# Kernel optimization log

Measured on AMD Instinct MI355X. Metric: run time of the kernel, lower is better.

## Reference

```python
import jax, jax.numpy as jnp
import numpy as np

N_NODES = 100000
N_EDGES = 1600000
IN_DIM = 128
OUT_DIM = 32
NUM_HEADS = 4


def setup_inputs() -> dict:
    key = jax.random.key(0)
    k1, k2, k3, k4, k5, k6 = jax.random.split(key, 6)
    feat = jax.random.normal(k1, (N_NODES, IN_DIM), dtype=jnp.float32)
    # xavier-uniform-ish scales
    fc_w = jax.random.normal(k2, (OUT_DIM * NUM_HEADS, IN_DIM), dtype=jnp.float32) * (1.0 / np.sqrt(IN_DIM))
    attn_src = jax.random.normal(k3, (1, NUM_HEADS, OUT_DIM), dtype=jnp.float32) * 0.1
    attn_dst = jax.random.normal(k4, (1, NUM_HEADS, OUT_DIM), dtype=jnp.float32) * 0.1
    src = jax.random.randint(k5, (N_EDGES,), 0, N_NODES, dtype=jnp.int64)
    dst = jax.random.randint(k6, (N_EDGES,), 0, N_NODES, dtype=jnp.int64)
    return {"feat": feat, "fc_w": fc_w, "attn_src": attn_src, "attn_dst": attn_dst, "src": src, "dst": dst}


def reference(feat, fc_w, attn_src, attn_dst, src, dst):
    N = feat.shape[0]
    # fc: [N, H*D] -> [N, H, D]
    h = (feat @ fc_w.T).reshape(N, NUM_HEADS, OUT_DIM)
    # per-node attention logits [N, H]
    e_src = jnp.sum(h * attn_src, axis=-1)
    e_dst = jnp.sum(h * attn_dst, axis=-1)
    # per-edge logits, LeakyReLU(0.2)  [E, H]
    e = e_src[src] + e_dst[dst]
    e = jnp.where(e > 0, e, 0.2 * e)
    # edge softmax over incoming edges of each dst node
    m = jax.ops.segment_max(e, dst, num_segments=N)          # [N, H], -inf for empty
    a = jnp.exp(e - m[dst])                                  # [E, H]
    s = jax.ops.segment_sum(a, dst, num_segments=N)          # [N, H]
    a = a / jnp.where(s[dst] > 0, s[dst], 1.0)
    # weighted scatter-sum aggregation: u_mul_e + sum
    msg = h[src] * a[:, :, None]                             # [E, H, D]
    out = jax.ops.segment_sum(msg, dst, num_segments=N)      # [N, H, D]
    h_out = out.reshape(N, NUM_HEADS * OUT_DIM)
    # residual: in_dim == out_dim*num_heads -> identity residual
    return h_out + feat
```

## Files before the change

### kernel.cpp

```cpp
#include <hip/hip_runtime.h>

#define HD 128
#define NHEADS 4
#define MBLK 128
#define APITCH 136

#define CHUNK_SHIFT 8
#define CHUNK_NODES 256
#define MAXCH 512
#define CLCAP 4352
#define PT_EDGES 4096
#define EPT 16
#define CAP 48

#define H8_SCALE   15.875f
#define H8_INVSCALE 0.062992126f

typedef __attribute__((ext_vector_type(8))) short bf16x8;
typedef __attribute__((ext_vector_type(4))) float f32x4;

__device__ __forceinline__ unsigned short f2bf(float x) {
    union { float f; unsigned u; } a; a.f = x;
    unsigned r = a.u + 0x7fffu + ((a.u >> 16) & 1u);
    return (unsigned short)(r >> 16);
}

__global__ __launch_bounds__(256) void partition_edges(
    const int* __restrict__ src, const int* __restrict__ dst,
    int* __restrict__ cursor,
    int2* __restrict__ clist,
    int2* __restrict__ spillP, int* __restrict__ nspillP,
    int E, int nchunks, int spillPCap)
{
    __shared__ int lcnt[MAXCH];
    __shared__ int gbase[MAXCH];
    const int tid = threadIdx.x;
    for (int i = tid; i < MAXCH; i += 256) lcnt[i] = 0;
    __syncthreads();

    const int e0 = blockIdx.x * PT_EDGES + tid;
    int d[EPT], s[EPT], r[EPT];
#pragma unroll
    for (int k = 0; k < EPT; k++) {
        int e = e0 + k * 256;
        d[k] = 0; s[k] = 0; r[k] = 0;
        if (e < E) { d[k] = dst[e]; s[k] = src[e]; }
    }
#pragma unroll
    for (int k = 0; k < EPT; k++) {
        int e = e0 + k * 256;
        if (e < E) r[k] = atomicAdd(&lcnt[d[k] >> CHUNK_SHIFT], 1);
    }
    __syncthreads();
    for (int c = tid; c < nchunks; c += 256) {
        int cnt = lcnt[c];
        gbase[c] = cnt ? atomicAdd(&cursor[c], cnt) : 0;
    }
    __syncthreads();
#pragma unroll
    for (int k = 0; k < EPT; k++) {
        int e = e0 + k * 256;
        if (e < E) {
            int c = d[k] >> CHUNK_SHIFT;
            int pos = gbase[c] + r[k];
            if (pos < CLCAP) {
                clist[(size_t)c * CLCAP + pos] = make_int2(d[k], s[k]);
            } else {
                int kk = atomicAdd(nspillP, 1);
                if (kk < spillPCap) spillP[kk] = make_int2(d[k], s[k]);
            }
        }
    }
}

__global__ __launch_bounds__(256) void bucketize(
    const int2* __restrict__ clist, const int* __restrict__ cursor,
    const int2* __restrict__ spillP, const int* __restrict__ nspillP,
    int* __restrict__ erec, int* __restrict__ counts,
    int2* __restrict__ spillB, int* __restrict__ nspillB,
    int N, int spillPCap, int spillBCap)
{
    __shared__ int lcnt[CHUNK_NODES];
    const int c = blockIdx.x;
    const int tid = threadIdx.x;
    lcnt[tid] = 0;
    __syncthreads();

    int cnt = cursor[c]; if (cnt > CLCAP) cnt = CLCAP;
    const int2* base = clist + (size_t)c * CLCAP;
    const int nodebase = c << CHUNK_SHIFT;

    for (int i = tid; i < cnt; i += 256) {
        int2 p = base[i];
        int pos = atomicAdd(&lcnt[p.x - nodebase], 1);
        if (pos < CAP) erec[(size_t)p.x * CAP + pos] = p.y;
        else { int kk = atomicAdd(nspillB, 1); if (kk < spillBCap) spillB[kk] = p; }
    }
    int nsp = *nspillP; if (nsp > spillPCap) nsp = spillPCap;
    for (int i = tid; i < nsp; i += 256) {
        int2 p = spillP[i];
        if ((p.x >> CHUNK_SHIFT) == c) {
            int pos = atomicAdd(&lcnt[p.x - nodebase], 1);
            if (pos < CAP) erec[(size_t)p.x * CAP + pos] = p.y;
            else { int kk = atomicAdd(nspillB, 1); if (kk < spillBCap) spillB[kk] = p; }
        }
    }
    __syncthreads();
    int n = nodebase + tid;
    if (n < N) counts[n] = lcnt[tid];
}

__global__ __launch_bounds__(256, 2) void gemm_mfma(
    const float* __restrict__ feat, const float* __restrict__ fc_w,
    const float* __restrict__ attn_src, const float* __restrict__ attn_dst,
    signed char* __restrict__ h8, float* __restrict__ e_src, float* __restrict__ e_dst,
    int N)
{
    __shared__ unsigned short As[MBLK * APITCH];
    __shared__ unsigned short Bs[HD * APITCH];
    const int tid = threadIdx.x;
    const int row0 = blockIdx.x * MBLK;

    for (int i = tid; i < 128 * 32; i += 256) {
        int o = i >> 5, j = i & 31;
        float4 v = ((const float4*)fc_w)[i];
        ushort4 u; u.x = f2bf(v.x); u.y = f2bf(v.y); u.z = f2bf(v.z); u.w = f2bf(v.w);
        *(ushort4*)&Bs[o * APITCH + j * 4] = u;
    }
    for (int i = tid; i < MBLK * 32; i += 256) {
        int r = i >> 5, j = i & 31;
        int rowg = row0 + r;
        float4 v = make_float4(0.f, 0.f, 0.f, 0.f);
        if (rowg < N) {
            v = ((const float4*)feat)[(size_t)rowg * 32 + j];
        }
        ushort4 u; u.x = f2bf(v.x); u.y = f2bf(v.y); u.z = f2bf(v.z); u.w = f2bf(v.w);
        *(ushort4*)&As[r * APITCH + j * 4] = u;
    }
    __syncthreads();

    const int w = tid >> 6, lane = tid & 63, quad = lane >> 4, lr = lane & 15;
    f32x4 acc[2][8];
#pragma unroll
    for (int rt = 0; rt < 2; rt++)
#pragma unroll
        for (int ct = 0; ct < 8; ct++) acc[rt][ct] = (f32x4){0.f, 0.f, 0.f, 0.f};

#pragma unroll
    for (int ks = 0; ks < 4; ks++) {
        const int k0 = ks * 32 + quad * 8;
        bf16x8 a0 = *(const bf16x8*)&As[(w * 32 + lr) * APITCH + k0];
        bf16x8 a1 = *(const bf16x8*)&As[(w * 32 + 16 + lr) * APITCH + k0];
        bf16x8 bf[8];
#pragma unroll
        for (int ct = 0; ct < 8; ct++)
            bf[ct] = *(const bf16x8*)&Bs[(ct * 16 + lr) * APITCH + k0];
#pragma unroll
        for (int ct = 0; ct < 8; ct++) {
            acc[0][ct] = __builtin_amdgcn_mfma_f32_16x16x32_bf16(a0, bf[ct], acc[0][ct], 0, 0, 0);
            acc[1][ct] = __builtin_amdgcn_mfma_f32_16x16x32_bf16(a1, bf[ct], acc[1][ct], 0, 0, 0);
        }
    }

#pragma unroll
    for (int rt = 0; rt < 2; rt++) {
#pragma unroll
        for (int ct = 0; ct < 8; ct++) {
            int col = ct * 16 + lr;
#pragma unroll
            for (int reg = 0; reg < 4; reg++) {
                int row = row0 + w * 32 + rt * 16 + quad * 4 + reg;
                if (row < N) {
                    float v = acc[rt][ct][reg];
                    v = fminf(fmaxf(v, -8.f), 8.f);
                    int q = (int)rintf(v * H8_SCALE);
                    h8[(size_t)row * 128 + col] = (signed char)q;
                }
            }
        }
    }

    float as_v[8], ad_v[8];
#pragma unroll
    for (int ct = 0; ct < 8; ct++) {
        as_v[ct] = attn_src[ct * 16 + lr];
        ad_v[ct] = attn_dst[ct * 16 + lr];
    }
#pragma unroll
    for (int rt = 0; rt < 2; rt++) {
#pragma unroll
        for (int reg = 0; reg < 4; reg++) {
            int row = row0 + w * 32 + rt * 16 + quad * 4 + reg;
            float ps[4], pd[4];
#pragma unroll
            for (int hd = 0; hd < 4; hd++) {
                ps[hd] = acc[rt][2 * hd][reg] * as_v[2 * hd] + acc[rt][2 * hd + 1][reg] * as_v[2 * hd + 1];
                pd[hd] = acc[rt][2 * hd][reg] * ad_v[2 * hd] + acc[rt][2 * hd + 1][reg] * ad_v[2 * hd + 1];
            }
#pragma unroll
            for (int off = 1; off < 16; off <<= 1) {
#pragma unroll
                for (int hd = 0; hd < 4; hd++) {
                    ps[hd] += __shfl_xor(ps[hd], off);
                    pd[hd] += __shfl_xor(pd[hd], off);
                }
            }
            if (lr == 0 && row < N) {
                *(float4*)&e_src[(size_t)row * 4] = make_float4(ps[0], ps[1], ps[2], ps[3]);
                *(float4*)&e_dst[(size_t)row * 4] = make_float4(pd[0], pd[1], pd[2], pd[3]);
            }
        }
    }
}

__global__ __launch_bounds__(256, 8) void node_agg(
    const int* __restrict__ erec, const int* __restrict__ counts,
    const signed char* __restrict__ h8,
    const float* __restrict__ e_src, const float* __restrict__ e_dst,
    const float* __restrict__ feat, float* __restrict__ out,
    const int2* __restrict__ spillB, const int* __restrict__ nspillB,
    int N, int spillBCap)
{
    const int lane  = threadIdx.x & 63;
    const int grp8  = lane >> 3;
    const int q     = lane & 7;
    const int head  = q >> 1;

    const int wgid   = (blockIdx.x * 256 + threadIdx.x) >> 6;
    const int nwaves = (gridDim.x * 256) >> 6;

    for (int nb0 = wgid * 8; nb0 < N; nb0 += nwaves * 8) {
        const int n = nb0 + grp8;
        const bool active = (n < N);
        const int deg = active ? counts[n] : 0;
        int md = deg;
        md = max(md, __shfl_xor(md, 8));
        md = max(md, __shfl_xor(md, 16));
        md = max(md, __shfl_xor(md, 32));
        if (md == 0) {
            if (active) {
                const float4* f = (const float4*)(feat + (size_t)n * HD) + q * 4;
                float4* o = (float4*)(out + (size_t)n * HD) + q * 4;
#pragma unroll
                for (int k = 0; k < 4; k++) o[k] = f[k];
            }
            continue;
        }
        const float ed = active ? e_dst[(size_t)n * 4 + head] : 0.f;
        const int fdeg = deg < CAP ? deg : CAP;
        const int mdc = md < CAP ? md : CAP;

        f32x4 a0 = (f32x4){0.f, 0.f, 0.f, 0.f};
        f32x4 a1 = (f32x4){0.f, 0.f, 0.f, 0.f};
        f32x4 a2 = (f32x4){0.f, 0.f, 0.f, 0.f};
        f32x4 a3 = (f32x4){0.f, 0.f, 0.f, 0.f};
        float s_l = 0.f;
#pragma unroll 4
        for (int j = 0; j < mdc; ++j) {
            float ev = 0.f; int si = 0;
            if (j < fdeg) {
                si = erec[(size_t)n * CAP + j];
                float v = e_src[(size_t)si * 4 + head] + ed;
                v = v > 0.f ? v : 0.2f * v;
                ev = __expf(v);
            }
            s_l += ev;
            const float evs = ev * H8_INVSCALE;
            uint4 hv = *(const uint4*)&h8[(size_t)si * 128 + q * 16];
            a0.x += evs * (float)(int)(signed char)(hv.x);
            a0.y += evs * (float)(int)(signed char)(hv.x >> 8);
            a0.z += evs * (float)(int)(signed char)(hv.x >> 16);
            a0.w += evs * (float)(int)(signed char)(hv.x >> 24);
            a1.x += evs * (float)(int)(signed char)(hv.y);
            a1.y += evs * (float)(int)(signed char)(hv.y >> 8);
            a1.z += evs * (float)(int)(signed char)(hv.y >> 16);
            a1.w += evs * (float)(int)(signed char)(hv.y >> 24);
            a2.x += evs * (float)(int)(signed char)(hv.z);
            a2.y += evs * (float)(int)(signed char)(hv.z >> 8);
            a2.z += evs * (float)(int)(signed char)(hv.z >> 16);
            a2.w += evs * (float)(int)(signed char)(hv.z >> 24);
            a3.x += evs * (float)(int)(signed char)(hv.w);
            a3.y += evs * (float)(int)(signed char)(hv.w >> 8);
            a3.z += evs * (float)(int)(signed char)(hv.w >> 16);
            a3.w += evs * (float)(int)(signed char)(hv.w >> 24);
        }
        if (__any(deg > CAP)) {
            int ns = *nspillB; if (ns > spillBCap) ns = spillBCap;
            for (int k = 0; k < ns; ++k) {
                int2 p = spillB[k];
                if (active && deg > CAP && p.x == n) {
                    int si = p.y;
                    float v = e_src[(size_t)si * 4 + head] + ed;
                    v = v > 0.f ? v : 0.2f * v;
                    float ev = __expf(v);
                    s_l += ev;
                    const float evs = ev * H8_INVSCALE;
                    uint4 hv = *(const uint4*)&h8[(size_t)si * 128 + q * 16];
                    a0.x += evs * (float)(int)(signed char)(hv.x);
                    a0.y += evs * (float)(int)(signed char)(hv.x >> 8);
                    a0.z += evs * (float)(int)(signed char)(hv.x >> 16);
                    a0.w += evs * (float)(int)(signed char)(hv.x >> 24);
                    a1.x += evs * (float)(int)(signed char)(hv.y);
                    a1.y += evs * (float)(int)(signed char)(hv.y >> 8);
                    a1.z += evs * (float)(int)(signed char)(hv.y >> 16);
                    a1.w += evs * (float)(int)(signed char)(hv.y >> 24);
                    a2.x += evs * (float)(int)(signed char)(hv.z);
                    a2.y += evs * (float)(int)(signed char)(hv.z >> 8);
                    a2.z += evs * (float)(int)(signed char)(hv.z >> 16);
                    a2.w += evs * (float)(int)(signed char)(hv.z >> 24);
                    a3.x += evs * (float)(int)(signed char)(hv.w);
                    a3.y += evs * (float)(int)(signed char)(hv.w >> 8);
                    a3.z += evs * (float)(int)(signed char)(hv.w >> 16);
                    a3.w += evs * (float)(int)(signed char)(hv.w >> 24);
                }
            }
        }
        if (active) {
            const float inv = (deg > 0) ? (1.0f / s_l) : 0.f;
            const float4* f = (const float4*)(feat + (size_t)n * HD) + q * 4;
            float4* o = (float4*)(out + (size_t)n * HD) + q * 4;
            float4 c0 = f[0], c1 = f[1], c2 = f[2], c3 = f[3];
            c0.x += a0.x * inv; c0.y += a0.y * inv; c0.z += a0.z * inv; c0.w += a0.w * inv;
            c1.x += a1.x * inv; c1.y += a1.y * inv; c1.z += a1.z * inv; c1.w += a1.w * inv;
            c2.x += a2.x * inv; c2.y += a2.y * inv; c2.z += a2.z * inv; c2.w += a2.w * inv;
            c3.x += a3.x * inv; c3.y += a3.y * inv; c3.z += a3.z * inv; c3.w += a3.w * inv;
            o[0] = c0; o[1] = c1; o[2] = c2; o[3] = c3;
        }
    }
}

extern "C" void kernel_launch(void* const* d_in, const int* in_sizes, int n_in,
                              void* d_out, int out_size, void* d_ws, size_t ws_size,
                              hipStream_t stream) {
    const float* feat     = (const float*)d_in[0];
    const float* fc_w     = (const float*)d_in[1];
    const float* attn_src = (const float*)d_in[2];
    const float* attn_dst = (const float*)d_in[3];
    const int*   src      = (const int*)d_in[4];
    const int*   dst      = (const int*)d_in[5];
    const int N = in_sizes[0] / HD;
    const int E = in_sizes[4];
    float* out = (float*)d_out;

    const int nchunks = (N + CHUNK_NODES - 1) >> CHUNK_SHIFT;
    const int spillPCap = E / 8;
    const int spillBCap = E / 8;

    signed char* h8 = (signed char*)d_ws;
    float* e_src  = (float*)(h8 + (size_t)N * HD);
    float* e_dst  = e_src + (size_t)N * NHEADS;
    int* erec     = (int*)(e_dst + (size_t)N * NHEADS);
    int* counts   = erec + (size_t)N * CAP;
    int* cursor   = counts + N;
    int* nspillP  = cursor + nchunks;
    int* nspillB  = nspillP + 1;
    int2* clist   = (int2*)(nspillB + 1);
    int2* spillP  = clist + (size_t)nchunks * CLCAP;
    int2* spillB  = spillP + spillPCap;

    const int npart = (E + PT_EDGES - 1) / PT_EDGES;

    hipMemsetAsync(cursor, 0, (size_t)(nchunks + 2) * sizeof(int), stream);
    partition_edges<<<npart, 256, 0, stream>>>(src, dst, cursor, clist, spillP, nspillP,
                                               E, nchunks, spillPCap);
    bucketize<<<nchunks, 256, 0, stream>>>(clist, cursor, spillP, nspillP,
                                           erec, counts, spillB, nspillB,
                                           N, spillPCap, spillBCap);
    gemm_mfma<<<(N + MBLK - 1) / MBLK, 256, 0, stream>>>(feat, fc_w, attn_src, attn_dst,
                                                         h8, e_src, e_dst, N);
    node_agg<<<2048, 256, 0, stream>>>(erec, counts, h8, e_src, e_dst, feat, out,
                                       spillB, nspillB, N, spillBCap);
}
```

Baseline: 272.2 us.

## Halve partition tile with LDS rank storage and widen bucketize to 512 threads

partition_edges now handles 2048 edges per block instead of 4096, doubling the block count. It keeps per-edge ranks in a shared-memory ushort array instead of registers, and reloads dst and src in the scatter phase instead of holding them in registers. bucketize now runs 512 threads per block and batches four loads before doing its atomics, to expose more memory-level parallelism across only about 391 blocks. The cost is re-reading the edge arrays, plus more global cursor atomics from the larger number of partition blocks.

```diff
diff --git a/kernel.cpp b/kernel.cpp
--- a/kernel.cpp
+++ b/kernel.cpp
@@ -9,8 +9,8 @@
 #define CHUNK_NODES 256
 #define MAXCH 512
 #define CLCAP 4352
-#define PT_EDGES 4096
-#define EPT 16
+#define PT_EDGES 2048
+#define EPT 8
 #define CAP 48
 
 #define H8_SCALE   15.875f
@@ -34,46 +34,49 @@
 {
     __shared__ int lcnt[MAXCH];
     __shared__ int gbase[MAXCH];
+    __shared__ unsigned short rnk[PT_EDGES];
     const int tid = threadIdx.x;
     for (int i = tid; i < MAXCH; i += 256) lcnt[i] = 0;
     __syncthreads();
 
-    const int e0 = blockIdx.x * PT_EDGES + tid;
-    int d[EPT], s[EPT], r[EPT];
+    const int ebase = blockIdx.x * PT_EDGES;
+
 #pragma unroll
     for (int k = 0; k < EPT; k++) {
-        int e = e0 + k * 256;
-        d[k] = 0; s[k] = 0; r[k] = 0;
-        if (e < E) { d[k] = dst[e]; s[k] = src[e]; }
-    }
-#pragma unroll
-    for (int k = 0; k < EPT; k++) {
-        int e = e0 + k * 256;
-        if (e < E) r[k] = atomicAdd(&lcnt[d[k] >> CHUNK_SHIFT], 1);
-    }
-    __syncthreads();
+        int idx = tid + k * 256;
+        int e = ebase + idx;
+        if (e < E) {
+            int d = dst[e];
+            rnk[idx] = (unsigned short)atomicAdd(&lcnt[d >> CHUNK_SHIFT], 1);
+        }
+    }
+    __syncthreads();
+
     for (int c = tid; c < nchunks; c += 256) {
         int cnt = lcnt[c];
         gbase[c] = cnt ? atomicAdd(&cursor[c], cnt) : 0;
     }
     __syncthreads();
+
 #pragma unroll
     for (int k = 0; k < EPT; k++) {
-        int e = e0 + k * 256;
+        int idx = tid + k * 256;
+        int e = ebase + idx;
         if (e < E) {
-            int c = d[k] >> CHUNK_SHIFT;
-            int pos = gbase[c] + r[k];
+            int d = dst[e], s = src[e];
+            int c = d >> CHUNK_SHIFT;
+            int pos = gbase[c] + (int)rnk[idx];
             if (pos < CLCAP) {
-                clist[(size_t)c * CLCAP + pos] = make_int2(d[k], s[k]);
+                clist[(size_t)c * CLCAP + pos] = make_int2(d, s);
             } else {
                 int kk = atomicAdd(nspillP, 1);
-                if (kk < spillPCap) spillP[kk] = make_int2(d[k], s[k]);
-            }
-        }
-    }
-}
-
-__global__ __launch_bounds__(256) void bucketize(
+                if (kk < spillPCap) spillP[kk] = make_int2(d, s);
+            }
+        }
+    }
+}
+
+__global__ __launch_bounds__(512) void bucketize(
     const int2* __restrict__ clist, const int* __restrict__ cursor,
     const int2* __restrict__ spillP, const int* __restrict__ nspillP,
     int* __restrict__ erec, int* __restrict__ counts,
@@ -83,21 +86,36 @@
     __shared__ int lcnt[CHUNK_NODES];
     const int c = blockIdx.x;
     const int tid = threadIdx.x;
-    lcnt[tid] = 0;
+    if (tid < CHUNK_NODES) lcnt[tid] = 0;
     __syncthreads();
 
     int cnt = cursor[c]; if (cnt > CLCAP) cnt = CLCAP;
     const int2* base = clist + (size_t)c * CLCAP;
     const int nodebase = c << CHUNK_SHIFT;
 
-    for (int i = tid; i < cnt; i += 256) {
-        int2 p = base[i];
-        int pos = atomicAdd(&lcnt[p.x - nodebase], 1);
-        if (pos < CAP) erec[(size_t)p.x * CAP + pos] = p.y;
-        else { int kk = atomicAdd(nspillB, 1); if (kk < spillBCap) spillB[kk] = p; }
+    for (int i0 = tid; i0 < cnt; i0 += 512 * 4) {
+        int2 p[4]; int pos[4];
+#pragma unroll
+        for (int k = 0; k < 4; k++) {
+            int i = i0 + k * 512;
+            p[k] = (i < cnt) ? base[i] : make_int2(nodebase, 0);
+        }
+#pragma unroll
+        for (int k = 0; k < 4; k++) {
+            int i = i0 + k * 512;
+            pos[k] = (i < cnt) ? atomicAdd(&lcnt[p[k].x - nodebase], 1) : CAP;
+        }
+#pragma unroll
+        for (int k = 0; k < 4; k++) {
+            int i = i0 + k * 512;
+            if (i < cnt) {
+                if (pos[k] < CAP) erec[(size_t)p[k].x * CAP + pos[k]] = p[k].y;
+                else { int kk = atomicAdd(nspillB, 1); if (kk < spillBCap) spillB[kk] = p[k]; }
+            }
+        }
     }
     int nsp = *nspillP; if (nsp > spillPCap) nsp = spillPCap;
-    for (int i = tid; i < nsp; i += 256) {
+    for (int i = tid; i < nsp; i += 512) {
         int2 p = spillP[i];
         if ((p.x >> CHUNK_SHIFT) == c) {
             int pos = atomicAdd(&lcnt[p.x - nodebase], 1);
@@ -106,8 +124,10 @@
         }
     }
     __syncthreads();
-    int n = nodebase + tid;
-    if (n < N) counts[n] = lcnt[tid];
+    if (tid < CHUNK_NODES) {
+        int n = nodebase + tid;
+        if (n < N) counts[n] = lcnt[tid];
+    }
 }
 
 __global__ __launch_bounds__(256, 2) void gemm_mfma(
@@ -363,7 +383,7 @@
     hipMemsetAsync(cursor, 0, (size_t)(nchunks + 2) * sizeof(int), stream);
     partition_edges<<<npart, 256, 0, stream>>>(src, dst, cursor, clist, spillP, nspillP,
                                                E, nchunks, spillPCap);
-    bucketize<<<nchunks, 256, 0, stream>>>(clist, cursor, spillP, nspillP,
+    bucketize<<<nchunks, 512, 0, stream>>>(clist, cursor, spillP, nspillP,
                                            erec, counts, spillB, nspillB,
                                            N, spillPCap, spillBCap);
     gemm_mfma<<<(N + MBLK - 1) / MBLK, 256, 0, stream>>>(feat, fc_w, attn_src, attn_dst,
```

After: 273.2 us. About the same (+0.4%).
